# Optimization experiments

Hardware: AMD Instinct MI355X
Metric: run time of the kernel (lower is better)

Reference implementation:

```python
import math
import jax, jax.numpy as jnp
import numpy as np

CHUNK_LEN = 64
NUM_HEADS = 16
HIDDEN = 1024
HEAD = HIDDEN // NUM_HEADS


def setup_inputs() -> dict:
    key = jax.random.key(0)
    ks = jax.random.split(key, 8)
    B, S, C, N, L = 4, 2048, 32, 2, 128
    scale = 1.0 / math.sqrt(HIDDEN)
    return {
        "query": jax.random.normal(ks[0], (B, S, HIDDEN), jnp.float32),
        "kv": jax.random.normal(ks[1], (B, C, N, L, HIDDEN), jnp.float32),
        "Wq": jax.random.normal(ks[2], (HIDDEN, HIDDEN), jnp.float32) * scale,
        "bq": jnp.zeros((HIDDEN,), jnp.float32),
        "Wk": jax.random.normal(ks[3], (HIDDEN, HIDDEN), jnp.float32) * scale,
        "bk": jnp.zeros((HIDDEN,), jnp.float32),
        "Wv": jax.random.normal(ks[4], (HIDDEN, HIDDEN), jnp.float32) * scale,
        "bv": jnp.zeros((HIDDEN,), jnp.float32),
    }


def reference(query, kv, Wq, bq, Wk, bk, Wv, bv):
    B, S, H = query.shape
    _, C, N, L, _ = kv.shape
    # shift query right by chunk_len-1 and pad to n_chunks*chunk_len
    q = query[:, CHUNK_LEN - 1:]
    add_len = C * CHUNK_LEN - q.shape[1]
    q = jnp.pad(q, ((0, 0), (0, add_len), (0, 0)))
    q = q.reshape(B, C, CHUNK_LEN, H)
    q = (q @ Wq.T + bq).reshape(B, C, CHUNK_LEN, NUM_HEADS, HEAD)
    k = (kv @ Wk.T + bk).reshape(B, C, N, L, NUM_HEADS, HEAD)
    v = (kv @ Wv.T + bv).reshape(B, C, N, L, NUM_HEADS, HEAD)
    # scores: [B, C, heads, chunk_len, N, L]
    attn = jnp.einsum("bcihd,bcnjhd->bchinj", q, k) / math.sqrt(HEAD)
    # softmax over flattened neighbor dims (n, j)
    attn = jax.nn.softmax(attn.reshape(B, C, NUM_HEADS, CHUNK_LEN, N * L), axis=-1)
    attn = attn.reshape(B, C, NUM_HEADS, CHUNK_LEN, N, L)
    h = jnp.einsum("bchinj,bcnjhd->bcihd", attn, v).reshape(B, C * CHUNK_LEN, H)
    # shift left: prepend chunk_len-1 zeros, truncate to seq_len
    h = jnp.pad(h, ((0, 0), (CHUNK_LEN - 1, 0), (0, 0)))[:, :S]
    return h
```

## Files before the change

### kernel.cpp

```cpp
#include <hip/hip_runtime.h>
#include <stdint.h>

#define HD 1024
#define SEQ 2048
#define NC 32

typedef __bf16 bf16x4 __attribute__((ext_vector_type(4)));
typedef __bf16 bf16x8 __attribute__((ext_vector_type(8)));
typedef float f32x4 __attribute__((ext_vector_type(4)));

__device__ inline unsigned short f2bf(float f) {
  union { float f; unsigned int u; } v; v.f = f;
  unsigned int r = v.u + 0x7fffu + ((v.u >> 16) & 1u);
  return (unsigned short)(r >> 16);
}
__device__ inline unsigned int pk2bf(float a, float b) {
  return (unsigned int)f2bf(a) | ((unsigned int)f2bf(b) << 16);
}
__device__ inline bf16x8 ld_frag8(const unsigned short* p) {
  bf16x4 lo = *(const bf16x4*)p;
  bf16x4 hi = *(const bf16x4*)(p + 4);
  return __builtin_shufflevector(lo, hi, 0, 1, 2, 3, 4, 5, 6, 7);
}
__device__ inline void glds16(const unsigned short* g, unsigned short* l) {
  __builtin_amdgcn_global_load_lds(
      (const __attribute__((address_space(1))) unsigned int*)g,
      (__attribute__((address_space(3))) unsigned int*)l, 16, 0, 0);
}

__global__ __launch_bounds__(256) void zero_head_kernel(float* __restrict__ out) {
  int i = (blockIdx.x * 256 + threadIdx.x) * 4;
  int b = i / 64512;
  int r = i - b * 64512;
  *(float4*)(out + (size_t)b * (SEQ * HD) + r) = make_float4(0.f, 0.f, 0.f, 0.f);
}

__global__ __launch_bounds__(256) void cvt_kernel(const float* __restrict__ in,
                                                  unsigned short* __restrict__ out, int n8) {
  int i = blockIdx.x * 256 + threadIdx.x;
  if (i < n8) {
    float4 a = ((const float4*)in)[(size_t)i * 2];
    float4 b = ((const float4*)in)[(size_t)i * 2 + 1];
    ((uint4*)out)[i] = make_uint4(pk2bf(a.x, a.y), pk2bf(a.z, a.w),
                                  pk2bf(b.x, b.y), pk2bf(b.z, b.w));
  }
}

__global__ __launch_bounds__(256) void cvt_q_kernel(const float* __restrict__ q,
                                                    unsigned short* __restrict__ out) {
  int i = blockIdx.x * 256 + threadIdx.x;
  int g = i >> 7, c8 = (i & 127) * 8;
  int b = g >> 11, tt = g & 2047;
  uint4 o = make_uint4(0, 0, 0, 0);
  if (tt < 1985) {
    const float* src = q + ((size_t)(b << 11) + tt + 63) * HD + c8;
    float4 a = *(const float4*)src;
    float4 bb = *(const float4*)(src + 4);
    o = make_uint4(pk2bf(a.x, a.y), pk2bf(a.z, a.w), pk2bf(bb.x, bb.y), pk2bf(bb.z, bb.w));
  }
  *(uint4*)(out + (size_t)g * HD + c8) = o;
}

__global__ __launch_bounds__(256, 2) void gemm_bf_kernel(
    const unsigned short* __restrict__ A, const unsigned short* __restrict__ W,
    const float* __restrict__ bias, unsigned short* __restrict__ Cout, int store_vt) {
  __shared__ unsigned short lds_a[128 * 32];
  __shared__ unsigned short lds_b[128 * 32];
  const int t = threadIdx.x;
  const int l = t & 63, w = t >> 6;
  const int wm = w >> 1, wn = w & 1;
  const int lr = l & 15, lq = l >> 4;
  const size_t arow0 = (size_t)blockIdx.y * 128;
  const size_t brow0 = (size_t)blockIdx.x * 128;
  const int c0 = t, c1 = 256 + t;
  const unsigned short* a0 = A + (arow0 + (c0 >> 2)) * HD + (c0 & 3) * 8;
  const unsigned short* a1 = A + (arow0 + (c1 >> 2)) * HD + (c1 & 3) * 8;
  const unsigned short* b0 = W + (brow0 + (c0 >> 2)) * HD + (c0 & 3) * 8;
  const unsigned short* b1 = W + (brow0 + (c1 >> 2)) * HD + (c1 & 3) * 8;

  f32x4 acc[4][4];
  for (int i = 0; i < 4; i++)
    for (int j = 0; j < 4; j++) acc[i][j] = (f32x4){0.f, 0.f, 0.f, 0.f};

  for (int kk = 0; kk < 32; ++kk) {
    const int k0 = kk * 32;
    __syncthreads();
    glds16(a0 + k0, lds_a + c0 * 8);
    glds16(a1 + k0, lds_a + c1 * 8);
    glds16(b0 + k0, lds_b + c0 * 8);
    glds16(b1 + k0, lds_b + c1 * 8);
    __syncthreads();
    bf16x8 af[4], bfr[4];
    for (int mt = 0; mt < 4; ++mt)
      af[mt] = *(const bf16x8*)(lds_a + (wm * 64 + mt * 16 + lr) * 32 + lq * 8);
    for (int nt = 0; nt < 4; ++nt)
      bfr[nt] = *(const bf16x8*)(lds_b + (wn * 64 + nt * 16 + lr) * 32 + lq * 8);
    for (int mt = 0; mt < 4; ++mt)
      for (int nt = 0; nt < 4; ++nt)
        acc[mt][nt] = __builtin_amdgcn_mfma_f32_16x16x32_bf16(af[mt], bfr[nt], acc[mt][nt], 0, 0, 0);
  }

  if (!store_vt) {
    for (int nt = 0; nt < 4; ++nt) {
      int n = blockIdx.x * 128 + wn * 64 + nt * 16 + lr;
      float bvv = bias[n];
      for (int mt = 0; mt < 4; ++mt) {
        size_t mbase = arow0 + wm * 64 + mt * 16 + lq * 4;
        for (int r = 0; r < 4; ++r)
          Cout[(mbase + r) * HD + n] = f2bf(acc[mt][nt][r] + bvv);
      }
    }
  } else {
    for (int nt = 0; nt < 4; ++nt) {
      int n = blockIdx.x * 128 + wn * 64 + nt * 16 + lr;
      float bvv = bias[n];
      int h = n >> 6, d = n & 63;
      for (int mt = 0; mt < 4; ++mt) {
        size_t m0 = arow0 + wm * 64 + mt * 16 + lq * 4;
        size_t bc = m0 >> 8, j = m0 & 255;
        *(ushort4*)(Cout + ((bc * 16 + h) * 64 + d) * 256 + j) =
            make_ushort4(f2bf(acc[mt][nt][0] + bvv), f2bf(acc[mt][nt][1] + bvv),
                         f2bf(acc[mt][nt][2] + bvv), f2bf(acc[mt][nt][3] + bvv));
      }
    }
  }
}

__global__ __launch_bounds__(256, 2) void gemm_f32_kernel(
    const float* __restrict__ A, const float* __restrict__ W,
    const float* __restrict__ bias, unsigned short* __restrict__ Cout,
    int store_vt, int qremap) {
  __shared__ unsigned short lds_a[128 * 32];
  __shared__ unsigned short lds_b[128 * 32];
  const int t = threadIdx.x;
  const int l = t & 63, w = t >> 6;
  const int wm = w >> 1, wn = w & 1;
  const int lr = l & 15, lq = l >> 4;
  const size_t arow0 = (size_t)blockIdx.y * 128;
  const size_t brow0 = (size_t)blockIdx.x * 128;

  f32x4 acc[4][4];
  for (int i = 0; i < 4; i++)
    for (int j = 0; j < 4; j++) acc[i][j] = (f32x4){0.f, 0.f, 0.f, 0.f};

  for (int kk = 0; kk < 32; ++kk) {
    const int k0 = kk * 32;
    uint4 av[2], bv[2];
    for (int p = 0; p < 2; ++p) {
      int chunk = p * 256 + t;
      int row = chunk >> 2, c8 = (chunk & 3) * 8;
      size_t grow = arow0 + row;
      bool valid = true;
      const float* srcA;
      if (qremap) {
        int bb = (int)(grow >> 11), tt = (int)(grow & 2047);
        valid = tt < 1985;
        srcA = A + ((size_t)(bb << 11) + tt + 63) * HD + k0 + c8;
      } else {
        srcA = A + grow * HD + k0 + c8;
      }
      if (valid) {
        float4 x = *(const float4*)srcA, y = *(const float4*)(srcA + 4);
        av[p] = make_uint4(pk2bf(x.x, x.y), pk2bf(x.z, x.w), pk2bf(y.x, y.y), pk2bf(y.z, y.w));
      } else av[p] = make_uint4(0, 0, 0, 0);
      const float* srcB = W + (brow0 + row) * HD + k0 + c8;
      float4 x = *(const float4*)srcB, y = *(const float4*)(srcB + 4);
      bv[p] = make_uint4(pk2bf(x.x, x.y), pk2bf(x.z, x.w), pk2bf(y.x, y.y), pk2bf(y.z, y.w));
    }
    __syncthreads();
    for (int p = 0; p < 2; ++p) {
      int chunk = p * 256 + t;
      *(uint4*)(lds_a + chunk * 8) = av[p];
      *(uint4*)(lds_b + chunk * 8) = bv[p];
    }
    __syncthreads();
    bf16x8 af[4], bfr[4];
    for (int mt = 0; mt < 4; ++mt)
      af[mt] = *(const bf16x8*)(lds_a + (wm * 64 + mt * 16 + lr) * 32 + lq * 8);
    for (int nt = 0; nt < 4; ++nt)
      bfr[nt] = *(const bf16x8*)(lds_b + (wn * 64 + nt * 16 + lr) * 32 + lq * 8);
    for (int mt = 0; mt < 4; ++mt)
      for (int nt = 0; nt < 4; ++nt)
        acc[mt][nt] = __builtin_amdgcn_mfma_f32_16x16x32_bf16(af[mt], bfr[nt], acc[mt][nt], 0, 0, 0);
  }

  if (!store_vt) {
    for (int nt = 0; nt < 4; ++nt) {
      int n = blockIdx.x * 128 + wn * 64 + nt * 16 + lr;
      float bvv = bias[n];
      for (int mt = 0; mt < 4; ++mt) {
        size_t mbase = arow0 + wm * 64 + mt * 16 + lq * 4;
        for (int r = 0; r < 4; ++r)
          Cout[(mbase + r) * HD + n] = f2bf(acc[mt][nt][r] + bvv);
      }
    }
  } else {
    for (int nt = 0; nt < 4; ++nt) {
      int n = blockIdx.x * 128 + wn * 64 + nt * 16 + lr;
      float bvv = bias[n];
      int h = n >> 6, d = n & 63;
      for (int mt = 0; mt < 4; ++mt) {
        size_t m0 = arow0 + wm * 64 + mt * 16 + lq * 4;
        size_t bc = m0 >> 8, j = m0 & 255;
        *(ushort4*)(Cout + ((bc * 16 + h) * 64 + d) * 256 + j) =
            make_ushort4(f2bf(acc[mt][nt][0] + bvv), f2bf(acc[mt][nt][1] + bvv),
                         f2bf(acc[mt][nt][2] + bvv), f2bf(acc[mt][nt][3] + bvv));
      }
    }
  }
}

#define QK_STRIDE 68
#define P_STRIDE 260

__global__ __launch_bounds__(256, 3) void attn_kernel(
    const unsigned short* __restrict__ Qp, const unsigned short* __restrict__ Kp,
    const unsigned short* __restrict__ Vt, float* __restrict__ out) {
  __shared__ unsigned short q_s[64 * QK_STRIDE];
  __shared__ unsigned short k_s[256 * QK_STRIDE];
  const int t = threadIdx.x;
  const int l = t & 63, w = t >> 6;
  const int lr = l & 15, lq = l >> 4;
  const int bid = blockIdx.x;
  const int head = bid & 15, cc = (bid >> 4) & 31, b = bid >> 9;
  const size_t qrow0 = (size_t)(b * NC + cc) * 64;
  const size_t kvrow0 = (size_t)(b * NC + cc) * 256;
  const int hcol = head * 64;
  const unsigned short* vbase = Vt + ((size_t)((b * NC + cc) * 16 + head) * 64) * 256;

  for (int p = 0; p < 4; ++p) {
    int chunk = p * 256 + t;
    int row = chunk >> 4, c4 = (chunk & 15) * 4;
    *(uint2*)(q_s + row * QK_STRIDE + c4) = *(const uint2*)(Qp + (qrow0 + row) * HD + hcol + c4);
  }
  for (int p = 0; p < 16; ++p) {
    int chunk = p * 256 + t;
    int row = chunk >> 4, c4 = (chunk & 15) * 4;
    *(uint2*)(k_s + row * QK_STRIDE + c4) = *(const uint2*)(Kp + (kvrow0 + row) * HD + hcol + c4);
  }
  __syncthreads();

  bf16x8 qa0 = ld_frag8(q_s + (w * 16 + lr) * QK_STRIDE + lq * 8);
  bf16x8 qa1 = ld_frag8(q_s + (w * 16 + lr) * QK_STRIDE + 32 + lq * 8);
  f32x4 sc[16];
  for (int nt = 0; nt < 16; ++nt) {
    bf16x8 kb0 = ld_frag8(k_s + (nt * 16 + lr) * QK_STRIDE + lq * 8);
    bf16x8 kb1 = ld_frag8(k_s + (nt * 16 + lr) * QK_STRIDE + 32 + lq * 8);
    f32x4 a = (f32x4){0.f, 0.f, 0.f, 0.f};
    a = __builtin_amdgcn_mfma_f32_16x16x32_bf16(qa0, kb0, a, 0, 0, 0);
    a = __builtin_amdgcn_mfma_f32_16x16x32_bf16(qa1, kb1, a, 0, 0, 0);
    sc[nt] = a;
  }
  float mrow[4] = {-1e30f, -1e30f, -1e30f, -1e30f};
  for (int nt = 0; nt < 16; ++nt)
    for (int r = 0; r < 4; ++r) mrow[r] = fmaxf(mrow[r], sc[nt][r]);
  for (int off = 1; off < 16; off <<= 1)
    for (int r = 0; r < 4; ++r) mrow[r] = fmaxf(mrow[r], __shfl_xor(mrow[r], off, 16));
  float srow[4] = {0.f, 0.f, 0.f, 0.f};
  const float cexp = 0.18033688011112042f;
  for (int nt = 0; nt < 16; ++nt)
    for (int r = 0; r < 4; ++r) {
      float p = exp2f((sc[nt][r] - mrow[r]) * cexp);
      sc[nt][r] = p;
      srow[r] += p;
    }
  for (int off = 1; off < 16; off <<= 1)
    for (int r = 0; r < 4; ++r) srow[r] += __shfl_xor(srow[r], off, 16);

  __syncthreads();

  for (int nt = 0; nt < 16; ++nt)
    for (int r = 0; r < 4; ++r)
      k_s[(w * 16 + lq * 4 + r) * P_STRIDE + nt * 16 + lr] = f2bf(sc[nt][r]);

  f32x4 o[4];
  for (int i = 0; i < 4; ++i) o[i] = (f32x4){0.f, 0.f, 0.f, 0.f};
  for (int ks = 0; ks < 8; ++ks) {
    bf16x8 pa = ld_frag8(k_s + (w * 16 + lr) * P_STRIDE + ks * 32 + lq * 8);
    for (int nt2 = 0; nt2 < 4; ++nt2) {
      bf16x8 vb = *(const bf16x8*)(vbase + (size_t)(nt2 * 16 + lr) * 256 + ks * 32 + lq * 8);
      o[nt2] = __builtin_amdgcn_mfma_f32_16x16x32_bf16(pa, vb, o[nt2], 0, 0, 0);
    }
  }

  for (int r = 0; r < 4; ++r) {
    int strip = w * 16 + lq * 4 + r;
    int trow = cc * 64 + strip;
    if (trow < 1985) {
      size_t orow = (size_t)b * SEQ + trow + 63;
      float inv = 1.0f / srow[r];
      for (int nt2 = 0; nt2 < 4; ++nt2)
        out[orow * HD + hcol + nt2 * 16 + lr] = o[nt2][r] * inv;
    }
  }
}

extern "C" void kernel_launch(void* const* d_in, const int* in_sizes, int n_in,
                              void* d_out, int out_size, void* d_ws, size_t ws_size,
                              hipStream_t stream) {
  (void)in_sizes; (void)n_in; (void)out_size;
  const float* query = (const float*)d_in[0];
  const float* kv    = (const float*)d_in[1];
  const float* Wq    = (const float*)d_in[2];
  const float* bq    = (const float*)d_in[3];
  const float* Wk    = (const float*)d_in[4];
  const float* bk    = (const float*)d_in[5];
  const float* Wv    = (const float*)d_in[6];
  const float* bv    = (const float*)d_in[7];
  float* out = (float*)d_out;

  unsigned short* Qp  = (unsigned short*)d_ws;
  unsigned short* Kp  = Qp + (size_t)8192 * 1024;
  unsigned short* Vt  = Kp + (size_t)32768 * 1024;
  unsigned short* Qbf = Vt + (size_t)32768 * 1024;
  unsigned short* KVb = Qbf + (size_t)8192 * 1024;
  unsigned short* Wqb = KVb + (size_t)32768 * 1024;
  unsigned short* Wkb = Wqb + (size_t)1024 * 1024;
  unsigned short* Wvb = Wkb + (size_t)1024 * 1024;
  const size_t need = ((size_t)8192 * 1024 * 2 + (size_t)32768 * 1024 * 2 + (size_t)1024 * 1024 * 3) * 2;
  const bool big = ws_size >= need;

  zero_head_kernel<<<dim3(252), dim3(256), 0, stream>>>(out);
  if (big) {
    cvt_q_kernel<<<dim3(4096), dim3(256), 0, stream>>>(query, Qbf);
    cvt_kernel<<<dim3(16384), dim3(256), 0, stream>>>(kv, KVb, 4194304);
    cvt_kernel<<<dim3(512), dim3(256), 0, stream>>>(Wq, Wqb, 131072);
    cvt_kernel<<<dim3(512), dim3(256), 0, stream>>>(Wk, Wkb, 131072);
    cvt_kernel<<<dim3(512), dim3(256), 0, stream>>>(Wv, Wvb, 131072);
    gemm_bf_kernel<<<dim3(8, 64), dim3(256), 0, stream>>>(Qbf, Wqb, bq, Qp, 0);
    gemm_bf_kernel<<<dim3(8, 256), dim3(256), 0, stream>>>(KVb, Wkb, bk, Kp, 0);
    gemm_bf_kernel<<<dim3(8, 256), dim3(256), 0, stream>>>(KVb, Wvb, bv, Vt, 1);
  } else {
    gemm_f32_kernel<<<dim3(8, 64), dim3(256), 0, stream>>>(query, Wq, bq, Qp, 0, 1);
    gemm_f32_kernel<<<dim3(8, 256), dim3(256), 0, stream>>>(kv, Wk, bk, Kp, 0, 0);
    gemm_f32_kernel<<<dim3(8, 256), dim3(256), 0, stream>>>(kv, Wv, bv, Vt, 1, 0);
  }
  attn_kernel<<<dim3(2048), dim3(256), 0, stream>>>(Qp, Kp, Vt, out);
}
```

Before: 519.6 us.

## Fuse activation fp32-to-bf16 conversion into GEMMs and compute K and V together

Removes the separate conversion passes for query and kv. The GEMMs now read fp32 activations directly and pack them to bf16 in registers before the LDS store, with weights still pre-converted. K and V projections are merged into one kernel that shares each A tile across two accumulator sets. Block indices are remapped so that blocks on the same XCD share A rows. This avoids a full extra read and write of the 128MB kv tensor, at the cost of doubled accumulator registers and synchronous fp32 loads in the inner loop.

Measured after the change: 535.9 us. 1.03x slower.

```diff
diff --git a/kernel.cpp b/kernel.cpp
--- a/kernel.cpp
+++ b/kernel.cpp
@@ -1,4 +1,5 @@
 #include <hip/hip_runtime.h>
+#include <hip/hip_bf16.h>
 #include <stdint.h>
 
 #define HD 1024
@@ -14,8 +15,13 @@
   unsigned int r = v.u + 0x7fffu + ((v.u >> 16) & 1u);
   return (unsigned short)(r >> 16);
 }
-__device__ inline unsigned int pk2bf(float a, float b) {
-  return (unsigned int)f2bf(a) | ((unsigned int)f2bf(b) << 16);
+__device__ inline unsigned int pkcvt(float a, float b) {
+  __hip_bfloat162 h = __float22bfloat162_rn(make_float2(a, b));
+  union { __hip_bfloat162 h; unsigned int u; } v; v.h = h;
+  return v.u;
+}
+__device__ inline uint4 pack8(float4 x, float4 y) {
+  return make_uint4(pkcvt(x.x, x.y), pkcvt(x.z, x.w), pkcvt(y.x, y.y), pkcvt(y.z, y.w));
 }
 __device__ inline bf16x8 ld_frag8(const unsigned short* p) {
   bf16x4 lo = *(const bf16x4*)p;
@@ -41,42 +47,108 @@
   if (i < n8) {
     float4 a = ((const float4*)in)[(size_t)i * 2];
     float4 b = ((const float4*)in)[(size_t)i * 2 + 1];
-    ((uint4*)out)[i] = make_uint4(pk2bf(a.x, a.y), pk2bf(a.z, a.w),
-                                  pk2bf(b.x, b.y), pk2bf(b.z, b.w));
-  }
-}
-
-__global__ __launch_bounds__(256) void cvt_q_kernel(const float* __restrict__ q,
-                                                    unsigned short* __restrict__ out) {
-  int i = blockIdx.x * 256 + threadIdx.x;
-  int g = i >> 7, c8 = (i & 127) * 8;
-  int b = g >> 11, tt = g & 2047;
-  uint4 o = make_uint4(0, 0, 0, 0);
-  if (tt < 1985) {
-    const float* src = q + ((size_t)(b << 11) + tt + 63) * HD + c8;
-    float4 a = *(const float4*)src;
-    float4 bb = *(const float4*)(src + 4);
-    o = make_uint4(pk2bf(a.x, a.y), pk2bf(a.z, a.w), pk2bf(bb.x, bb.y), pk2bf(bb.z, bb.w));
-  }
-  *(uint4*)(out + (size_t)g * HD + c8) = o;
-}
-
-__global__ __launch_bounds__(256, 2) void gemm_bf_kernel(
-    const unsigned short* __restrict__ A, const unsigned short* __restrict__ W,
-    const float* __restrict__ bias, unsigned short* __restrict__ Cout, int store_vt) {
+    ((uint4*)out)[i] = pack8(a, b);
+  }
+}
+
+__global__ __launch_bounds__(256, 2) void gemm_kv_kernel(
+    const float* __restrict__ A, const unsigned short* __restrict__ Wkb,
+    const unsigned short* __restrict__ Wvb, const float* __restrict__ bk,
+    const float* __restrict__ bv, unsigned short* __restrict__ Kp,
+    unsigned short* __restrict__ Vt) {
+  __shared__ unsigned short lds_a[128 * 32];
+  __shared__ unsigned short lds_bk[128 * 32];
+  __shared__ unsigned short lds_bv[128 * 32];
+  const int t = threadIdx.x;
+  const int l = t & 63, w = t >> 6;
+  const int wm = w >> 1, wn = w & 1;
+  const int lr = l & 15, lq = l >> 4;
+  const int bid = blockIdx.x;
+  const int xcd = bid & 7, local = bid >> 3;
+  const int nblk = local & 7, mblk = xcd * 32 + (local >> 3);
+  const size_t arow0 = (size_t)mblk * 128;
+  const size_t brow0 = (size_t)nblk * 128;
+  const int c0 = t, c1 = 256 + t;
+  const float* a0 = A + (arow0 + (c0 >> 2)) * HD + (c0 & 3) * 8;
+  const float* a1 = A + (arow0 + (c1 >> 2)) * HD + (c1 & 3) * 8;
+  const unsigned short* bk0 = Wkb + (brow0 + (c0 >> 2)) * HD + (c0 & 3) * 8;
+  const unsigned short* bk1 = Wkb + (brow0 + (c1 >> 2)) * HD + (c1 & 3) * 8;
+  const unsigned short* bv0 = Wvb + (brow0 + (c0 >> 2)) * HD + (c0 & 3) * 8;
+  const unsigned short* bv1 = Wvb + (brow0 + (c1 >> 2)) * HD + (c1 & 3) * 8;
+
+  f32x4 acck[4][4], accv[4][4];
+  for (int i = 0; i < 4; i++)
+    for (int j = 0; j < 4; j++) {
+      acck[i][j] = (f32x4){0.f, 0.f, 0.f, 0.f};
+      accv[i][j] = (f32x4){0.f, 0.f, 0.f, 0.f};
+    }
+
+  for (int kk = 0; kk < 32; ++kk) {
+    const int k0 = kk * 32;
+    __syncthreads();
+    glds16(bk0 + k0, lds_bk + c0 * 8);
+    glds16(bk1 + k0, lds_bk + c1 * 8);
+    glds16(bv0 + k0, lds_bv + c0 * 8);
+    glds16(bv1 + k0, lds_bv + c1 * 8);
+    {
+      float4 x0 = *(const float4*)(a0 + k0), y0 = *(const float4*)(a0 + k0 + 4);
+      float4 x1 = *(const float4*)(a1 + k0), y1 = *(const float4*)(a1 + k0 + 4);
+      *(uint4*)(lds_a + c0 * 8) = pack8(x0, y0);
+      *(uint4*)(lds_a + c1 * 8) = pack8(x1, y1);
+    }
+    __syncthreads();
+    bf16x8 af[4], bkf[4], bvf[4];
+    for (int mt = 0; mt < 4; ++mt)
+      af[mt] = *(const bf16x8*)(lds_a + (wm * 64 + mt * 16 + lr) * 32 + lq * 8);
+    for (int nt = 0; nt < 4; ++nt) {
+      bkf[nt] = *(const bf16x8*)(lds_bk + (wn * 64 + nt * 16 + lr) * 32 + lq * 8);
+      bvf[nt] = *(const bf16x8*)(lds_bv + (wn * 64 + nt * 16 + lr) * 32 + lq * 8);
+    }
+    for (int mt = 0; mt < 4; ++mt)
+      for (int nt = 0; nt < 4; ++nt) {
+        acck[mt][nt] = __builtin_amdgcn_mfma_f32_16x16x32_bf16(af[mt], bkf[nt], acck[mt][nt], 0, 0, 0);
+        accv[mt][nt] = __builtin_amdgcn_mfma_f32_16x16x32_bf16(af[mt], bvf[nt], accv[mt][nt], 0, 0, 0);
+      }
+  }
+
+  for (int nt = 0; nt < 4; ++nt) {
+    int n = nblk * 128 + wn * 64 + nt * 16 + lr;
+    float bkk = bk[n], bvv = bv[n];
+    int h = n >> 6, d = n & 63;
+    for (int mt = 0; mt < 4; ++mt) {
+      size_t mbase = arow0 + wm * 64 + mt * 16 + lq * 4;
+      for (int r = 0; r < 4; ++r)
+        Kp[(mbase + r) * HD + n] = f2bf(acck[mt][nt][r] + bkk);
+      size_t bc = mbase >> 8, j = mbase & 255;
+      *(ushort4*)(Vt + ((bc * 16 + h) * 64 + d) * 256 + j) =
+          make_ushort4(f2bf(accv[mt][nt][0] + bvv), f2bf(accv[mt][nt][1] + bvv),
+                       f2bf(accv[mt][nt][2] + bvv), f2bf(accv[mt][nt][3] + bvv));
+    }
+  }
+}
+
+__global__ __launch_bounds__(256, 2) void gemm_q_kernel(
+    const float* __restrict__ A, const unsigned short* __restrict__ Wqb,
+    const float* __restrict__ bq, unsigned short* __restrict__ Qp) {
   __shared__ unsigned short lds_a[128 * 32];
   __shared__ unsigned short lds_b[128 * 32];
   const int t = threadIdx.x;
   const int l = t & 63, w = t >> 6;
   const int wm = w >> 1, wn = w & 1;
   const int lr = l & 15, lq = l >> 4;
-  const size_t arow0 = (size_t)blockIdx.y * 128;
-  const size_t brow0 = (size_t)blockIdx.x * 128;
+  const int bid = blockIdx.x;
+  const int xcd = bid & 7, local = bid >> 3;
+  const int nblk = local & 7, mblk = xcd * 8 + (local >> 3);
+  const size_t arow0 = (size_t)mblk * 128;
+  const size_t brow0 = (size_t)nblk * 128;
   const int c0 = t, c1 = 256 + t;
-  const unsigned short* a0 = A + (arow0 + (c0 >> 2)) * HD + (c0 & 3) * 8;
-  const unsigned short* a1 = A + (arow0 + (c1 >> 2)) * HD + (c1 & 3) * 8;
-  const unsigned short* b0 = W + (brow0 + (c0 >> 2)) * HD + (c0 & 3) * 8;
-  const unsigned short* b1 = W + (brow0 + (c1 >> 2)) * HD + (c1 & 3) * 8;
+  const unsigned short* b0 = Wqb + (brow0 + (c0 >> 2)) * HD + (c0 & 3) * 8;
+  const unsigned short* b1 = Wqb + (brow0 + (c1 >> 2)) * HD + (c1 & 3) * 8;
+  size_t g0 = arow0 + (c0 >> 2), g1 = arow0 + (c1 >> 2);
+  int t0 = (int)(g0 & 2047), t1 = (int)(g1 & 2047);
+  bool v0 = t0 < 1985, v1 = t1 < 1985;
+  const float* a0 = A + ((g0 & ~(size_t)2047) + t0 + 63) * HD + (c0 & 3) * 8;
+  const float* a1 = A + ((g1 & ~(size_t)2047) + t1 + 63) * HD + (c1 & 3) * 8;
 
   f32x4 acc[4][4];
   for (int i = 0; i < 4; i++)
@@ -85,10 +157,15 @@
   for (int kk = 0; kk < 32; ++kk) {
     const int k0 = kk * 32;
     __syncthreads();
-    glds16(a0 + k0, lds_a + c0 * 8);
-    glds16(a1 + k0, lds_a + c1 * 8);
     glds16(b0 + k0, lds_b + c0 * 8);
     glds16(b1 + k0, lds_b + c1 * 8);
+    {
+      uint4 p0 = make_uint4(0, 0, 0, 0), p1 = make_uint4(0, 0, 0, 0);
+      if (v0) p0 = pack8(*(const float4*)(a0 + k0), *(const float4*)(a0 + k0 + 4));
+      if (v1) p1 = pack8(*(const float4*)(a1 + k0), *(const float4*)(a1 + k0 + 4));
+      *(uint4*)(lds_a + c0 * 8) = p0;
+      *(uint4*)(lds_a + c1 * 8) = p1;
+    }
     __syncthreads();
     bf16x8 af[4], bfr[4];
     for (int mt = 0; mt < 4; ++mt)
@@ -100,112 +177,13 @@
         acc[mt][nt] = __builtin_amdgcn_mfma_f32_16x16x32_bf16(af[mt], bfr[nt], acc[mt][nt], 0, 0, 0);
   }
 
-  if (!store_vt) {
-    for (int nt = 0; nt < 4; ++nt) {
-      int n = blockIdx.x * 128 + wn * 64 + nt * 16 + lr;
-      float bvv = bias[n];
-      for (int mt = 0; mt < 4; ++mt) {
-        size_t mbase = arow0 + wm * 64 + mt * 16 + lq * 4;
-        for (int r = 0; r < 4; ++r)
-          Cout[(mbase + r) * HD + n] = f2bf(acc[mt][nt][r] + bvv);
-      }
-    }
-  } else {
-    for (int nt = 0; nt < 4; ++nt) {
-      int n = blockIdx.x * 128 + wn * 64 + nt * 16 + lr;
-      float bvv = bias[n];
-      int h = n >> 6, d = n & 63;
-      for (int mt = 0; mt < 4; ++mt) {
-        size_t m0 = arow0 + wm * 64 + mt * 16 + lq * 4;
-        size_t bc = m0 >> 8, j = m0 & 255;
-        *(ushort4*)(Cout + ((bc * 16 + h) * 64 + d) * 256 + j) =
-            make_ushort4(f2bf(acc[mt][nt][0] + bvv), f2bf(acc[mt][nt][1] + bvv),
-                         f2bf(acc[mt][nt][2] + bvv), f2bf(acc[mt][nt][3] + bvv));
-      }
-    }
-  }
-}
-
-__global__ __launch_bounds__(256, 2) void gemm_f32_kernel(
-    const float* __restrict__ A, const float* __restrict__ W,
-    const float* __restrict__ bias, unsigned short* __restrict__ Cout,
-    int store_vt, int qremap) {
-  __shared__ unsigned short lds_a[128 * 32];
-  __shared__ unsigned short lds_b[128 * 32];
-  const int t = threadIdx.x;
-  const int l = t & 63, w = t >> 6;
-  const int wm = w >> 1, wn = w & 1;
-  const int lr = l & 15, lq = l >> 4;
-  const size_t arow0 = (size_t)blockIdx.y * 128;
-  const size_t brow0 = (size_t)blockIdx.x * 128;
-
-  f32x4 acc[4][4];
-  for (int i = 0; i < 4; i++)
-    for (int j = 0; j < 4; j++) acc[i][j] = (f32x4){0.f, 0.f, 0.f, 0.f};
-
-  for (int kk = 0; kk < 32; ++kk) {
-    const int k0 = kk * 32;
-    uint4 av[2], bv[2];
-    for (int p = 0; p < 2; ++p) {
-      int chunk = p * 256 + t;
-      int row = chunk >> 2, c8 = (chunk & 3) * 8;
-      size_t grow = arow0 + row;
-      bool valid = true;
-      const float* srcA;
-      if (qremap) {
-        int bb = (int)(grow >> 11), tt = (int)(grow & 2047);
-        valid = tt < 1985;
-        srcA = A + ((size_t)(bb << 11) + tt + 63) * HD + k0 + c8;
-      } else {
-        srcA = A + grow * HD + k0 + c8;
-      }
-      if (valid) {
-        float4 x = *(const float4*)srcA, y = *(const float4*)(srcA + 4);
-        av[p] = make_uint4(pk2bf(x.x, x.y), pk2bf(x.z, x.w), pk2bf(y.x, y.y), pk2bf(y.z, y.w));
-      } else av[p] = make_uint4(0, 0, 0, 0);
-      const float* srcB = W + (brow0 + row) * HD + k0 + c8;
-      float4 x = *(const float4*)srcB, y = *(const float4*)(srcB + 4);
-      bv[p] = make_uint4(pk2bf(x.x, x.y), pk2bf(x.z, x.w), pk2bf(y.x, y.y), pk2bf(y.z, y.w));
-    }
-    __syncthreads();
-    for (int p = 0; p < 2; ++p) {
-      int chunk = p * 256 + t;
-      *(uint4*)(lds_a + chunk * 8) = av[p];
-      *(uint4*)(lds_b + chunk * 8) = bv[p];
-    }
-    __syncthreads();
-    bf16x8 af[4], bfr[4];
-    for (int mt = 0; mt < 4; ++mt)
-      af[mt] = *(const bf16x8*)(lds_a + (wm * 64 + mt * 16 + lr) * 32 + lq * 8);
-    for (int nt = 0; nt < 4; ++nt)
-      bfr[nt] = *(const bf16x8*)(lds_b + (wn * 64 + nt * 16 + lr) * 32 + lq * 8);
-    for (int mt = 0; mt < 4; ++mt)
-      for (int nt = 0; nt < 4; ++nt)
-        acc[mt][nt] = __builtin_amdgcn_mfma_f32_16x16x32_bf16(af[mt], bfr[nt], acc[mt][nt], 0, 0, 0);
-  }
-
-  if (!store_vt) {
-    for (int nt = 0; nt < 4; ++nt) {
-      int n = blockIdx.x * 128 + wn * 64 + nt * 16 + lr;
-      float bvv = bias[n];
-      for (int mt = 0; mt < 4; ++mt) {
-        size_t mbase = arow0 + wm * 64 + mt * 16 + lq * 4;
-        for (int r = 0; r < 4; ++r)
-          Cout[(mbase + r) * HD + n] = f2bf(acc[mt][nt][r] + bvv);
-      }
-    }
-  } else {
-    for (int nt = 0; nt < 4; ++nt) {
-      int n = blockIdx.x * 128 + wn * 64 + nt * 16 + lr;
-      float bvv = bias[n];
-      int h = n >> 6, d = n & 63;
-      for (int mt = 0; mt < 4; ++mt) {
-        size_t m0 = arow0 + wm * 64 + mt * 16 + lq * 4;
-        size_t bc = m0 >> 8, j = m0 & 255;
-        *(ushort4*)(Cout + ((bc * 16 + h) * 64 + d) * 256 + j) =
-            make_ushort4(f2bf(acc[mt][nt][0] + bvv), f2bf(acc[mt][nt][1] + bvv),
-                         f2bf(acc[mt][nt][2] + bvv), f2bf(acc[mt][nt][3] + bvv));
-      }
+  for (int nt = 0; nt < 4; ++nt) {
+    int n = nblk * 128 + wn * 64 + nt * 16 + lr;
+    float bvv = bq[n];
+    for (int mt = 0; mt < 4; ++mt) {
+      size_t mbase = arow0 + wm * 64 + mt * 16 + lq * 4;
+      for (int r = 0; r < 4; ++r)
+        Qp[(mbase + r) * HD + n] = f2bf(acc[mt][nt][r] + bvv);
     }
   }
 }
@@ -298,7 +276,7 @@
 extern "C" void kernel_launch(void* const* d_in, const int* in_sizes, int n_in,
                               void* d_out, int out_size, void* d_ws, size_t ws_size,
                               hipStream_t stream) {
-  (void)in_sizes; (void)n_in; (void)out_size;
+  (void)in_sizes; (void)n_in; (void)out_size; (void)ws_size;
   const float* query = (const float*)d_in[0];
   const float* kv    = (const float*)d_in[1];
   const float* Wq    = (const float*)d_in[2];
@@ -312,28 +290,15 @@
   unsigned short* Qp  = (unsigned short*)d_ws;
   unsigned short* Kp  = Qp + (size_t)8192 * 1024;
   unsigned short* Vt  = Kp + (size_t)32768 * 1024;
-  unsigned short* Qbf = Vt + (size_t)32768 * 1024;
-  unsigned short* KVb = Qbf + (size_t)8192 * 1024;
-  unsigned short* Wqb = KVb + (size_t)32768 * 1024;
+  unsigned short* Wqb = Vt + (size_t)32768 * 1024;
   unsigned short* Wkb = Wqb + (size_t)1024 * 1024;
   unsigned short* Wvb = Wkb + (size_t)1024 * 1024;
-  const size_t need = ((size_t)8192 * 1024 * 2 + (size_t)32768 * 1024 * 2 + (size_t)1024 * 1024 * 3) * 2;
-  const bool big = ws_size >= need;
 
   zero_head_kernel<<<dim3(252), dim3(256), 0, stream>>>(out);
-  if (big) {
-    cvt_q_kernel<<<dim3(4096), dim3(256), 0, stream>>>(query, Qbf);
-    cvt_kernel<<<dim3(16384), dim3(256), 0, stream>>>(kv, KVb, 4194304);
-    cvt_kernel<<<dim3(512), dim3(256), 0, stream>>>(Wq, Wqb, 131072);
-    cvt_kernel<<<dim3(512), dim3(256), 0, stream>>>(Wk, Wkb, 131072);
-    cvt_kernel<<<dim3(512), dim3(256), 0, stream>>>(Wv, Wvb, 131072);
-    gemm_bf_kernel<<<dim3(8, 64), dim3(256), 0, stream>>>(Qbf, Wqb, bq, Qp, 0);
-    gemm_bf_kernel<<<dim3(8, 256), dim3(256), 0, stream>>>(KVb, Wkb, bk, Kp, 0);
-    gemm_bf_kernel<<<dim3(8, 256), dim3(256), 0, stream>>>(KVb, Wvb, bv, Vt, 1);
-  } else {
-    gemm_f32_kernel<<<dim3(8, 64), dim3(256), 0, stream>>>(query, Wq, bq, Qp, 0, 1);
-    gemm_f32_kernel<<<dim3(8, 256), dim3(256), 0, stream>>>(kv, Wk, bk, Kp, 0, 0);
-    gemm_f32_kernel<<<dim3(8, 256), dim3(256), 0, stream>>>(kv, Wv, bv, Vt, 1, 0);
-  }
+  cvt_kernel<<<dim3(512), dim3(256), 0, stream>>>(Wq, Wqb, 131072);
+  cvt_kernel<<<dim3(512), dim3(256), 0, stream>>>(Wk, Wkb, 131072);
+  cvt_kernel<<<dim3(512), dim3(256), 0, stream>>>(Wv, Wvb, 131072);
+  gemm_q_kernel<<<dim3(512), dim3(256), 0, stream>>>(query, Wqb, bq, Qp);
+  gemm_kv_kernel<<<dim3(2048), dim3(256), 0, stream>>>(kv, Wkb, Wvb, bk, bv, Kp, Vt);
   attn_kernel<<<dim3(2048), dim3(256), 0, stream>>>(Qp, Kp, Vt, out);
 }
```
